# Optimization experiments

Hardware: AMD Instinct MI355X
Metric: run time of the kernel (lower is better)

Reference implementation:

```python
import jax, jax.numpy as jnp
import numpy as np

B, N, C, H = 2, 2048, 768, 12
D = C // H  # head dim = 64


def _rotate_half(x):
    d2 = x.shape[-1] // 2
    x1, x2 = x[..., :d2], x[..., d2:]
    return jnp.concatenate([-x2, x1], axis=-1)


def _apply_rope(x, sin, cos):
    # x: [B,H,N,D], sin/cos: [N,D] -> broadcast over (B,H)
    return x * cos[None, None] + _rotate_half(x) * sin[None, None]


def setup_inputs() -> dict:
    key = jax.random.key(0)
    ks = jax.random.split(key, 7)
    x = jax.random.normal(ks[0], (B, N, C), dtype=jnp.float32)
    sin_spatial = jax.random.normal(ks[1], (N, D), dtype=jnp.float32)
    cos_spatial = jax.random.normal(ks[2], (N, D), dtype=jnp.float32)
    s = 1.0 / np.sqrt(C)
    W_qkv = jax.random.uniform(ks[3], (C, 3 * C), jnp.float32, -s, s)
    b_qkv = jax.random.uniform(ks[4], (3 * C,), jnp.float32, -s, s)
    W_out = jax.random.uniform(ks[5], (C, C), jnp.float32, -s, s)
    b_out = jax.random.uniform(ks[6], (C,), jnp.float32, -s, s)
    return {"x": x, "sin_spatial": sin_spatial, "cos_spatial": cos_spatial,
            "W_qkv": W_qkv, "b_qkv": b_qkv, "W_out": W_out, "b_out": b_out}


def reference(x, sin_spatial, cos_spatial, W_qkv, b_qkv, W_out, b_out):
    qkv = x @ W_qkv + b_qkv                       # [B,N,3C]
    qkv = qkv.reshape(B, N, 3, H, D).transpose(2, 0, 3, 1, 4)  # [3,B,H,N,D]
    q, k, v = qkv[0], qkv[1], qkv[2]
    q = _apply_rope(q, sin_spatial, cos_spatial)
    k = _apply_rope(k, sin_spatial, cos_spatial)
    att = jnp.einsum('bhqd,bhkd->bhqk', q, k) * (D ** -0.5)
    att = jax.nn.softmax(att, axis=-1)            # dropout is identity (eval)
    y = jnp.einsum('bhqk,bhkd->bhqd', att, v)     # [B,H,N,D]
    y = y.transpose(0, 2, 1, 3).reshape(B, N, C)
    return y @ W_out + b_out
```

## Files before the change

### kernel.cpp

```cpp
#include <hip/hip_runtime.h>
#include <hip/hip_bf16.h>

#define BB 2
#define NN 2048
#define CC 768
#define HH 12
#define DD 64
#define MM 4096
#define N3 2304

typedef __attribute__((ext_vector_type(8))) short bf16x8;
typedef __attribute__((ext_vector_type(4))) float f32x4;

#define QSCALE 0.18033688011112043f


__device__ __forceinline__ unsigned short f2bf(float f) {
    union { float f; unsigned u; } v; v.f = f;
    unsigned r = v.u + 0x7FFFu + ((v.u >> 16) & 1u);
    return (unsigned short)(r >> 16);
}

__device__ __forceinline__ short f2bf_rn(float f) {
    union { __hip_bfloat16 h; short s; } v;
    v.h = __float2bfloat16(f);
    return v.s;
}

__device__ __forceinline__ float exp2_hw(float x) {
    float r;
    asm("v_exp_f32 %0, %1" : "=v"(r) : "v"(x));
    return r;
}

__device__ __forceinline__ bf16x8 ld_frag(const unsigned short* p) {
    bf16x8 r;
    __builtin_memcpy(&r, p, 8);
    __builtin_memcpy((char*)&r + 8, p + 16, 8);
    return r;
}

__device__ __forceinline__ bf16x8 ld_frag16(const unsigned short* p) {
    bf16x8 r;
    __builtin_memcpy(&r, p, 16);
    return r;
}

__global__ void k_cvt(const float* __restrict__ s, unsigned short* __restrict__ d, int n4) {
    int i = blockIdx.x * blockDim.x + threadIdx.x;
    int st = gridDim.x * blockDim.x;
    for (; i < n4; i += st) {
        float4 v = ((const float4*)s)[i];
        ushort4 o;
        o.x = f2bf(v.x); o.y = f2bf(v.y); o.z = f2bf(v.z); o.w = f2bf(v.w);
        ((ushort4*)d)[i] = o;
    }
}

__global__ void k_cvtT(const float* __restrict__ s, unsigned short* __restrict__ d,
                       int R, int Cc) {
    __shared__ unsigned short t[64][72];
    const int c0 = blockIdx.x * 64, r0 = blockIdx.y * 64;
    const int tr = threadIdx.x >> 4;
    const int tc = (threadIdx.x & 15) * 4;
#pragma unroll
    for (int i = 0; i < 4; i++) {
        int r = tr + i * 16;
        float4 v = *(const float4*)(s + (size_t)(r0 + r) * Cc + c0 + tc);
        t[tc + 0][r] = f2bf(v.x);
        t[tc + 1][r] = f2bf(v.y);
        t[tc + 2][r] = f2bf(v.z);
        t[tc + 3][r] = f2bf(v.w);
    }
    __syncthreads();
    const int wr = threadIdx.x >> 2;
    const int wc = (threadIdx.x & 3) * 16;
    *(uint4*)(d + (size_t)(c0 + wr) * R + r0 + wc)     = *(uint4*)&t[wr][wc];
    *(uint4*)(d + (size_t)(c0 + wr) * R + r0 + wc + 8) = *(uint4*)&t[wr][wc + 8];
}

__launch_bounds__(256)
__global__ void k_qkv(const unsigned short* __restrict__ xb,
                      const unsigned short* __restrict__ wt,
                      const float* __restrict__ bias,
                      const float* __restrict__ sinp,
                      const float* __restrict__ cosp,
                      unsigned short* __restrict__ qws,
                      unsigned short* __restrict__ kws,
                      unsigned short* __restrict__ vws) {
    __shared__ unsigned short As[128][40];
    __shared__ unsigned short Bs[64][40];
    const int tid = threadIdx.x;
    const int lane = tid & 63, w = tid >> 6;
    const int ql = lane & 15, lg = lane >> 4;
    const int row0 = blockIdx.x * 128;
    const int j0 = blockIdx.y * 64;

    f32x4 acc[2][4];
#pragma unroll
    for (int a = 0; a < 2; a++)
#pragma unroll
        for (int b = 0; b < 4; b++) acc[a][b] = f32x4{0.f, 0.f, 0.f, 0.f};

    const int ar = tid >> 1, ac = (tid & 1) * 16;
    const int jr = tid >> 2, kc = (tid & 3) * 8;

    for (int k0 = 0; k0 < CC; k0 += 32) {
        uint4 av0 = *(const uint4*)(xb + (size_t)(row0 + ar) * CC + k0 + ac);
        uint4 av1 = *(const uint4*)(xb + (size_t)(row0 + ar) * CC + k0 + ac + 8);
        uint4 bv  = *(const uint4*)(wt + (size_t)(j0 + jr) * CC + k0 + kc);
        *(uint4*)&As[ar][ac]     = av0;
        *(uint4*)&As[ar][ac + 8] = av1;
        *(uint4*)&Bs[jr][kc]     = bv;
        __syncthreads();

        bf16x8 af[2], bfr[4];
#pragma unroll
        for (int fr = 0; fr < 2; fr++) af[fr] = ld_frag(&As[w * 32 + fr * 16 + ql][lg * 4]);
#pragma unroll
        for (int fn = 0; fn < 4; fn++) bfr[fn] = ld_frag(&Bs[fn * 16 + ql][lg * 4]);
#pragma unroll
        for (int fr = 0; fr < 2; fr++)
#pragma unroll
            for (int fn = 0; fn < 4; fn++)
                acc[fr][fn] = __builtin_amdgcn_mfma_f32_16x16x32_bf16(af[fr], bfr[fn], acc[fr][fn], 0, 0, 0);
        __syncthreads();
    }

    float vals[2][4][4];
#pragma unroll
    for (int fr = 0; fr < 2; fr++)
#pragma unroll
        for (int fn = 0; fn < 4; fn++) {
            float bj = bias[j0 + fn * 16 + ql];
#pragma unroll
            for (int r = 0; r < 4; r++) vals[fr][fn][r] = acc[fr][fn][r] + bj;
        }
    const int t = j0 / CC;
    const int h = (j0 % CC) >> 6;
    if (t < 2) {
        unsigned short* outp = (t == 0) ? qws : kws;
        const float qs = (t == 0) ? QSCALE : 1.0f;
#pragma unroll
        for (int fr = 0; fr < 2; fr++)
#pragma unroll
            for (int r = 0; r < 4; r++) {
                int m = row0 + w * 32 + fr * 16 + lg * 4 + r;
                int b = m >> 11, n = m & (NN - 1);
#pragma unroll
                for (int fn = 0; fn < 4; fn++) {
                    int d = fn * 16 + ql;
                    float cv = cosp[n * DD + d], sv = sinp[n * DD + d];
                    float other = vals[fr][fn ^ 2][r];
                    float rv = (vals[fr][fn][r] * cv + ((fn < 2) ? -other : other) * sv) * qs;
                    int dcol = (t == 0) ? d
                             : ((fn >> 1) * 32 + (ql >> 2) * 8 + (fn & 1) * 4 + (ql & 3));
                    outp[((size_t)(b * HH + h) * NN + n) * DD + dcol] = f2bf(rv);
                }
            }
    } else {
#pragma unroll
        for (int fr = 0; fr < 2; fr++)
#pragma unroll
            for (int r = 0; r < 4; r++) {
                int m = row0 + w * 32 + fr * 16 + lg * 4 + r;
                int b = m >> 11, n = m & (NN - 1);
                int ncol = (n & ~31) + lg * 8 + (fr & 1) * 4 + r;
#pragma unroll
                for (int fn = 0; fn < 4; fn++) {
                    int d = fn * 16 + ql;
                    vws[((size_t)(b * HH + h) * DD + d) * NN + ncol] = f2bf(vals[fr][fn][r]);
                }
            }
    }
}

__launch_bounds__(128)
__global__ void k_attn(const unsigned short* __restrict__ qws,
                       const unsigned short* __restrict__ kws,
                       const unsigned short* __restrict__ vws,
                       unsigned short* __restrict__ yws) {
    __shared__ unsigned short Ks[2][64][72];
    __shared__ unsigned short Vs[2][64][72];
    const int tid = threadIdx.x;
    const int lane = tid & 63, w = tid >> 6;
    const int ql = lane & 15, lg = lane >> 4;
    const int d0 = blockIdx.x;
    const int bh = (d0 & 7) + 8 * (d0 >> 8);
    const int qb = (d0 >> 3) & 31;
    const int qw = qb * 64 + w * 32;
    const unsigned short* Qp = qws + (size_t)bh * NN * DD;
    const unsigned short* Kp = kws + (size_t)bh * NN * DD;
    const unsigned short* Vp = vws + (size_t)bh * DD * NN;

    bf16x8 qf[2][2];
#pragma unroll
    for (int fn = 0; fn < 2; fn++)
#pragma unroll
        for (int kb = 0; kb < 2; kb++)
            qf[fn][kb] = ld_frag(Qp + (size_t)(qw + fn * 16 + ql) * DD + kb * 32 + lg * 4);

    f32x4 oacc[4][2];
#pragma unroll
    for (int a = 0; a < 4; a++)
#pragma unroll
        for (int b = 0; b < 2; b++) oacc[a][b] = f32x4{0.f, 0.f, 0.f, 0.f};
    float mrun[2] = {-1e30f, -1e30f}, lrun[2] = {0.f, 0.f};

    const int srow = tid >> 1;
    const int shalf = (tid & 1) * 32;

#pragma unroll
    for (int j = 0; j < 4; j++) {
        *(uint4*)&Ks[0][srow][shalf + j * 8] = *(const uint4*)(Kp + (size_t)srow * DD + shalf + j * 8);
        *(uint4*)&Vs[0][srow][shalf + j * 8] = *(const uint4*)(Vp + (size_t)srow * NN + shalf + j * 8);
    }
    __syncthreads();

    const int NT = NN / 64;
    int cur = 0;
    for (int kt = 0; kt < NT; kt++) {
        uint4 kn[4], vn[4];
        const bool hasn = (kt + 1 < NT);
        if (hasn) {
#pragma unroll
            for (int j = 0; j < 4; j++) {
                kn[j] = *(const uint4*)(Kp + (size_t)((kt + 1) * 64 + srow) * DD + shalf + j * 8);
                vn[j] = *(const uint4*)(Vp + (size_t)srow * NN + (kt + 1) * 64 + shalf + j * 8);
            }
        }
        const unsigned short (*Kc)[72] = Ks[cur];
        const unsigned short (*Vc)[72] = Vs[cur];

        f32x4 sacc[4][2];
#pragma unroll
        for (int a = 0; a < 4; a++)
#pragma unroll
            for (int b = 0; b < 2; b++) sacc[a][b] = f32x4{0.f, 0.f, 0.f, 0.f};
        __builtin_amdgcn_s_setprio(1);
#pragma unroll
        for (int kb = 0; kb < 2; kb++) {
            bf16x8 kf[4];
#pragma unroll
            for (int fr = 0; fr < 4; fr++)
                kf[fr] = ld_frag16(&Kc[fr * 16 + ql][kb * 32 + lg * 8]);
#pragma unroll
            for (int fr = 0; fr < 4; fr++)
#pragma unroll
                for (int fn = 0; fn < 2; fn++)
                    sacc[fr][fn] = __builtin_amdgcn_mfma_f32_16x16x32_bf16(kf[fr], qf[fn][kb], sacc[fr][fn], 0, 0, 0);
        }
        __builtin_amdgcn_s_setprio(0);

        bf16x8 pB[2][2];
#pragma unroll
        for (int fn = 0; fn < 2; fn++) {
            float ma = fmaxf(fmaxf(sacc[0][fn][0], sacc[0][fn][1]), fmaxf(sacc[0][fn][2], sacc[0][fn][3]));
            float mb = fmaxf(fmaxf(sacc[1][fn][0], sacc[1][fn][1]), fmaxf(sacc[1][fn][2], sacc[1][fn][3]));
            float mc = fmaxf(fmaxf(sacc[2][fn][0], sacc[2][fn][1]), fmaxf(sacc[2][fn][2], sacc[2][fn][3]));
            float md = fmaxf(fmaxf(sacc[3][fn][0], sacc[3][fn][1]), fmaxf(sacc[3][fn][2], sacc[3][fn][3]));
            float tm = fmaxf(fmaxf(ma, mb), fmaxf(mc, md));
            tm = fmaxf(tm, __shfl_xor(tm, 16));
            tm = fmaxf(tm, __shfl_xor(tm, 32));
            if (__any(tm > mrun[fn] + 8.0f)) {
                float mn = fmaxf(mrun[fn], tm);
                float scl = exp2_hw(mrun[fn] - mn);
                lrun[fn] *= scl;
#pragma unroll
                for (int db = 0; db < 4; db++) oacc[db][fn] *= scl;
                mrun[fn] = mn;
            }
            float ts = 0.f;
#pragma unroll
            for (int fr = 0; fr < 4; fr++)
#pragma unroll
                for (int r = 0; r < 4; r++) {
                    float p = exp2_hw(sacc[fr][fn][r] - mrun[fn]);
                    sacc[fr][fn][r] = p;
                    ts += p;
                }
            ts += __shfl_xor(ts, 16);
            ts += __shfl_xor(ts, 32);
            lrun[fn] += ts;

#pragma unroll
            for (int kkb = 0; kkb < 2; kkb++) {
                bf16x8 t8;
#pragma unroll
                for (int e = 0; e < 8; e++)
                    t8[e] = f2bf_rn(sacc[kkb * 2 + (e >> 2)][fn][e & 3]);
                pB[fn][kkb] = t8;
            }
        }

        __builtin_amdgcn_s_setprio(1);
#pragma unroll
        for (int db = 0; db < 4; db++) {
            bf16x8 va[2];
#pragma unroll
            for (int kkb = 0; kkb < 2; kkb++)
                va[kkb] = ld_frag16(&Vc[db * 16 + ql][kkb * 32 + lg * 8]);
#pragma unroll
            for (int kkb = 0; kkb < 2; kkb++)
#pragma unroll
                for (int fn = 0; fn < 2; fn++)
                    oacc[db][fn] = __builtin_amdgcn_mfma_f32_16x16x32_bf16(va[kkb], pB[fn][kkb], oacc[db][fn], 0, 0, 0);
        }
        __builtin_amdgcn_s_setprio(0);

        if (hasn) {
#pragma unroll
            for (int j = 0; j < 4; j++) {
                *(uint4*)&Ks[cur ^ 1][srow][shalf + j * 8] = kn[j];
                *(uint4*)&Vs[cur ^ 1][srow][shalf + j * 8] = vn[j];
            }
            __syncthreads();
            cur ^= 1;
        }
    }

    const int b = bh / HH, h = bh % HH;
#pragma unroll
    for (int fn = 0; fn < 2; fn++) {
        float inv = 1.0f / lrun[fn];
        int q = qw + fn * 16 + ql;
        unsigned short* yp = yws + (size_t)(b * NN + q) * CC + h * DD + lg * 4;
#pragma unroll
        for (int db = 0; db < 4; db++) {
            ushort4 o;
            o.x = f2bf(oacc[db][fn][0] * inv);
            o.y = f2bf(oacc[db][fn][1] * inv);
            o.z = f2bf(oacc[db][fn][2] * inv);
            o.w = f2bf(oacc[db][fn][3] * inv);
            *(ushort4*)(yp + db * 16) = o;
        }
    }
}

__launch_bounds__(256)
__global__ void k_out(const unsigned short* __restrict__ yb,
                      const unsigned short* __restrict__ wt,
                      const float* __restrict__ bias,
                      float* __restrict__ out) {
    __shared__ unsigned short As[128][40];
    __shared__ unsigned short Bs[64][40];
    const int tid = threadIdx.x;
    const int lane = tid & 63, w = tid >> 6;
    const int ql = lane & 15, lg = lane >> 4;
    const int row0 = blockIdx.x * 128;
    const int j0 = blockIdx.y * 64;

    f32x4 acc[2][4];
#pragma unroll
    for (int a = 0; a < 2; a++)
#pragma unroll
        for (int b = 0; b < 4; b++) acc[a][b] = f32x4{0.f, 0.f, 0.f, 0.f};

    const int ar = tid >> 1, ac = (tid & 1) * 16;
    const int jr = tid >> 2, kc = (tid & 3) * 8;

    for (int k0 = 0; k0 < CC; k0 += 32) {
        uint4 av0 = *(const uint4*)(yb + (size_t)(row0 + ar) * CC + k0 + ac);
        uint4 av1 = *(const uint4*)(yb + (size_t)(row0 + ar) * CC + k0 + ac + 8);
        uint4 bv  = *(const uint4*)(wt + (size_t)(j0 + jr) * CC + k0 + kc);
        *(uint4*)&As[ar][ac]     = av0;
        *(uint4*)&As[ar][ac + 8] = av1;
        *(uint4*)&Bs[jr][kc]     = bv;
        __syncthreads();

        bf16x8 af[2], bfr[4];
#pragma unroll
        for (int fr = 0; fr < 2; fr++) af[fr] = ld_frag(&As[w * 32 + fr * 16 + ql][lg * 4]);
#pragma unroll
        for (int fn = 0; fn < 4; fn++) bfr[fn] = ld_frag(&Bs[fn * 16 + ql][lg * 4]);
#pragma unroll
        for (int fr = 0; fr < 2; fr++)
#pragma unroll
            for (int fn = 0; fn < 4; fn++)
                acc[fr][fn] = __builtin_amdgcn_mfma_f32_16x16x32_bf16(af[fr], bfr[fn], acc[fr][fn], 0, 0, 0);
        __syncthreads();
    }

#pragma unroll
    for (int fr = 0; fr < 2; fr++)
#pragma unroll
        for (int fn = 0; fn < 4; fn++) {
            float bj = bias[j0 + fn * 16 + ql];
#pragma unroll
            for (int r = 0; r < 4; r++) {
                int m = row0 + w * 32 + fr * 16 + lg * 4 + r;
                out[(size_t)m * CC + j0 + fn * 16 + ql] = acc[fr][fn][r] + bj;
            }
        }
}

extern "C" void kernel_launch(void* const* d_in, const int* in_sizes, int n_in,
                              void* d_out, int out_size, void* d_ws, size_t ws_size,
                              hipStream_t stream) {
    const float* x    = (const float*)d_in[0];
    const float* sinp = (const float*)d_in[1];
    const float* cosp = (const float*)d_in[2];
    const float* wqkv = (const float*)d_in[3];
    const float* bqkv = (const float*)d_in[4];
    const float* wout = (const float*)d_in[5];
    const float* bout = (const float*)d_in[6];
    float* out = (float*)d_out;
    char* ws = (char*)d_ws;

    unsigned short* xb  = (unsigned short*)(ws);
    unsigned short* wqb = (unsigned short*)(ws + 6291456);
    unsigned short* wob = (unsigned short*)(ws + 9830400);
    unsigned short* qws = (unsigned short*)(ws + 11010048);
    unsigned short* kws = (unsigned short*)(ws + 17301504);
    unsigned short* vws = (unsigned short*)(ws + 23592960);
    unsigned short* yws = (unsigned short*)(ws + 29884416);
    if (ws_size < 36175872) return;

    k_cvt<<<dim3(512), dim3(256), 0, stream>>>(x, xb, MM * CC / 4);
    k_cvtT<<<dim3(36, 12), dim3(256), 0, stream>>>(wqkv, wqb, CC, N3);
    k_cvtT<<<dim3(12, 12), dim3(256), 0, stream>>>(wout, wob, CC, CC);
    k_qkv<<<dim3(32, 36), dim3(256), 0, stream>>>(xb, wqb, bqkv, sinp, cosp, qws, kws, vws);
    k_attn<<<dim3(768), dim3(128), 0, stream>>>(qws, kws, vws, yws);
    k_out<<<dim3(32, 12), dim3(256), 0, stream>>>(yws, wob, bout, out);
}
```

Measured before the change: 136.3 us.

## Split attention KV range across two wave pairs and merge partial softmax

The attention block grows from 128 to 256 threads. Each pair of waves handles half of the key/value sequence for the same 64 queries, and the two partial results (m, l, O) are merged through shared memory at the end, flash-decoding style. This doubles the waves per block and halves each wave's serial loop length, aiming for more latency hiding on a 768-block grid. In exchange the per-half K/V double buffering is gone, so each tile load now sits between two barriers, and the merge step adds shared-memory traffic and extra syncs.

```diff
diff --git a/kernel.cpp b/kernel.cpp
--- a/kernel.cpp
+++ b/kernel.cpp
@@ -175,24 +175,27 @@
     }
 }
 
-__launch_bounds__(128)
+__launch_bounds__(256, 3)
 __global__ void k_attn(const unsigned short* __restrict__ qws,
                        const unsigned short* __restrict__ kws,
                        const unsigned short* __restrict__ vws,
                        unsigned short* __restrict__ yws) {
-    __shared__ unsigned short Ks[2][64][72];
-    __shared__ unsigned short Vs[2][64][72];
+    __shared__ __align__(16) unsigned short SM[4 * 64 * 72];
     const int tid = threadIdx.x;
     const int lane = tid & 63, w = tid >> 6;
     const int ql = lane & 15, lg = lane >> 4;
+    const int qgrp = w & 1, khalf = w >> 1;
     const int d0 = blockIdx.x;
     const int bh = (d0 & 7) + 8 * (d0 >> 8);
     const int qb = (d0 >> 3) & 31;
-    const int qw = qb * 64 + w * 32;
+    const int qw = qb * 64 + qgrp * 32;
     const unsigned short* Qp = qws + (size_t)bh * NN * DD;
     const unsigned short* Kp = kws + (size_t)bh * NN * DD;
     const unsigned short* Vp = vws + (size_t)bh * DD * NN;
 
+    unsigned short* Kc = SM + khalf * (64 * 72);
+    unsigned short* Vc = SM + (2 + khalf) * (64 * 72);
+
     bf16x8 qf[2][2];
 #pragma unroll
     for (int fn = 0; fn < 2; fn++)
@@ -207,30 +210,30 @@
         for (int b = 0; b < 2; b++) oacc[a][b] = f32x4{0.f, 0.f, 0.f, 0.f};
     float mrun[2] = {-1e30f, -1e30f}, lrun[2] = {0.f, 0.f};
 
-    const int srow = tid >> 1;
-    const int shalf = (tid & 1) * 32;
+    const int htid = tid & 127;
+    const int srow = htid >> 1;
+    const int shalf = (htid & 1) * 32;
 
 #pragma unroll
     for (int j = 0; j < 4; j++) {
-        *(uint4*)&Ks[0][srow][shalf + j * 8] = *(const uint4*)(Kp + (size_t)srow * DD + shalf + j * 8);
-        *(uint4*)&Vs[0][srow][shalf + j * 8] = *(const uint4*)(Vp + (size_t)srow * NN + shalf + j * 8);
+        *(uint4*)&Kc[srow * 72 + shalf + j * 8] =
+            *(const uint4*)(Kp + (size_t)(khalf * 1024 + srow) * DD + shalf + j * 8);
+        *(uint4*)&Vc[srow * 72 + shalf + j * 8] =
+            *(const uint4*)(Vp + (size_t)srow * NN + khalf * 1024 + shalf + j * 8);
     }
     __syncthreads();
 
-    const int NT = NN / 64;
-    int cur = 0;
-    for (int kt = 0; kt < NT; kt++) {
+    for (int t = 0; t < 16; t++) {
+        const int g = khalf * 16 + t;
         uint4 kn[4], vn[4];
-        const bool hasn = (kt + 1 < NT);
+        const bool hasn = (t + 1 < 16);
         if (hasn) {
 #pragma unroll
             for (int j = 0; j < 4; j++) {
-                kn[j] = *(const uint4*)(Kp + (size_t)((kt + 1) * 64 + srow) * DD + shalf + j * 8);
-                vn[j] = *(const uint4*)(Vp + (size_t)srow * NN + (kt + 1) * 64 + shalf + j * 8);
-            }
-        }
-        const unsigned short (*Kc)[72] = Ks[cur];
-        const unsigned short (*Vc)[72] = Vs[cur];
+                kn[j] = *(const uint4*)(Kp + (size_t)((g + 1) * 64 + srow) * DD + shalf + j * 8);
+                vn[j] = *(const uint4*)(Vp + (size_t)srow * NN + (g + 1) * 64 + shalf + j * 8);
+            }
+        }
 
         f32x4 sacc[4][2];
 #pragma unroll
@@ -243,7 +246,7 @@
             bf16x8 kf[4];
 #pragma unroll
             for (int fr = 0; fr < 4; fr++)
-                kf[fr] = ld_frag16(&Kc[fr * 16 + ql][kb * 32 + lg * 8]);
+                kf[fr] = ld_frag16(&Kc[(fr * 16 + ql) * 72 + kb * 32 + lg * 8]);
 #pragma unroll
             for (int fr = 0; fr < 4; fr++)
 #pragma unroll
@@ -299,7 +302,7 @@
             bf16x8 va[2];
 #pragma unroll
             for (int kkb = 0; kkb < 2; kkb++)
-                va[kkb] = ld_frag16(&Vc[db * 16 + ql][kkb * 32 + lg * 8]);
+                va[kkb] = ld_frag16(&Vc[(db * 16 + ql) * 72 + kkb * 32 + lg * 8]);
 #pragma unroll
             for (int kkb = 0; kkb < 2; kkb++)
 #pragma unroll
@@ -309,30 +312,54 @@
         __builtin_amdgcn_s_setprio(0);
 
         if (hasn) {
+            __syncthreads();
 #pragma unroll
             for (int j = 0; j < 4; j++) {
-                *(uint4*)&Ks[cur ^ 1][srow][shalf + j * 8] = kn[j];
-                *(uint4*)&Vs[cur ^ 1][srow][shalf + j * 8] = vn[j];
+                *(uint4*)&Kc[srow * 72 + shalf + j * 8] = kn[j];
+                *(uint4*)&Vc[srow * 72 + shalf + j * 8] = vn[j];
             }
             __syncthreads();
-            cur ^= 1;
-        }
-    }
-
-    const int b = bh / HH, h = bh % HH;
-#pragma unroll
-    for (int fn = 0; fn < 2; fn++) {
-        float inv = 1.0f / lrun[fn];
-        int q = qw + fn * 16 + ql;
-        unsigned short* yp = yws + (size_t)(b * NN + q) * CC + h * DD + lg * 4;
-#pragma unroll
-        for (int db = 0; db < 4; db++) {
-            ushort4 o;
-            o.x = f2bf(oacc[db][fn][0] * inv);
-            o.y = f2bf(oacc[db][fn][1] * inv);
-            o.z = f2bf(oacc[db][fn][2] * inv);
-            o.w = f2bf(oacc[db][fn][3] * inv);
-            *(ushort4*)(yp + db * 16) = o;
+        }
+    }
+
+    __syncthreads();
+    float* ex = (float*)SM;
+    const int exb = (qgrp * 64 + lane) * 37;
+    if (khalf == 1) {
+#pragma unroll
+        for (int fn = 0; fn < 2; fn++)
+#pragma unroll
+            for (int db = 0; db < 4; db++)
+#pragma unroll
+                for (int r = 0; r < 4; r++)
+                    ex[exb + fn * 16 + db * 4 + r] = oacc[db][fn][r];
+        ex[exb + 32] = mrun[0];
+        ex[exb + 33] = mrun[1];
+        ex[exb + 34] = lrun[0];
+        ex[exb + 35] = lrun[1];
+    }
+    __syncthreads();
+    if (khalf == 0) {
+        const int b = bh / HH, h = bh % HH;
+#pragma unroll
+        for (int fn = 0; fn < 2; fn++) {
+            float m1 = ex[exb + 32 + fn];
+            float l1 = ex[exb + 34 + fn];
+            float M  = fmaxf(mrun[fn], m1);
+            float e0 = exp2_hw(mrun[fn] - M);
+            float e1 = exp2_hw(m1 - M);
+            float inv = 1.0f / (lrun[fn] * e0 + l1 * e1);
+            int q = qw + fn * 16 + ql;
+            unsigned short* yp = yws + (size_t)(b * NN + q) * CC + h * DD + lg * 4;
+#pragma unroll
+            for (int db = 0; db < 4; db++) {
+                ushort4 o;
+                o.x = f2bf((oacc[db][fn][0] * e0 + ex[exb + fn * 16 + db * 4 + 0] * e1) * inv);
+                o.y = f2bf((oacc[db][fn][1] * e0 + ex[exb + fn * 16 + db * 4 + 1] * e1) * inv);
+                o.z = f2bf((oacc[db][fn][2] * e0 + ex[exb + fn * 16 + db * 4 + 2] * e1) * inv);
+                o.w = f2bf((oacc[db][fn][3] * e0 + ex[exb + fn * 16 + db * 4 + 3] * e1) * inv);
+                *(ushort4*)(yp + db * 16) = o;
+            }
         }
     }
 }
@@ -420,6 +447,6 @@
     k_cvtT<<<dim3(36, 12), dim3(256), 0, stream>>>(wqkv, wqb, CC, N3);
     k_cvtT<<<dim3(12, 12), dim3(256), 0, stream>>>(wout, wob, CC, CC);
     k_qkv<<<dim3(32, 36), dim3(256), 0, stream>>>(xb, wqb, bqkv, sinp, cosp, qws, kws, vws);
-    k_attn<<<dim3(768), dim3(128), 0, stream>>>(qws, kws, vws, yws);
+    k_attn<<<dim3(768), dim3(256), 0, stream>>>(qws, kws, vws, yws);
     k_out<<<dim3(32, 12), dim3(256), 0, stream>>>(yws, wob, bout, out);
 }
```

New measurement: 198.4 us. 1.46x slower.

## Run attention blocks as single waves with one K/V LDS buffer and no barriers

Applied to the files above, without the earlier changes.

The attention kernel changes from two-wave blocks with a double-buffered K/V tile in LDS to one-wave blocks. Each wave stages the whole 64-row K and V tile itself through a single LDS buffer, and the grid doubles to 1536 blocks. Because a wave's own LDS reads and writes stay in program order, the __syncthreads barrier is removed and LDS use per block drops. The trade-off is that each wave now loads the full K/V tile on its own, so global/L2 traffic for K/V doubles and the 16 prefetch registers per thread may raise register pressure.

```diff
diff --git a/kernel.cpp b/kernel.cpp
--- a/kernel.cpp
+++ b/kernel.cpp
@@ -175,20 +175,19 @@
     }
 }
 
-__launch_bounds__(128)
+__launch_bounds__(64)
 __global__ void k_attn(const unsigned short* __restrict__ qws,
                        const unsigned short* __restrict__ kws,
                        const unsigned short* __restrict__ vws,
                        unsigned short* __restrict__ yws) {
-    __shared__ unsigned short Ks[2][64][72];
-    __shared__ unsigned short Vs[2][64][72];
-    const int tid = threadIdx.x;
-    const int lane = tid & 63, w = tid >> 6;
+    __shared__ __align__(16) unsigned short Ks[64][72];
+    __shared__ __align__(16) unsigned short Vs[64][72];
+    const int lane = threadIdx.x;
     const int ql = lane & 15, lg = lane >> 4;
     const int d0 = blockIdx.x;
-    const int bh = (d0 & 7) + 8 * (d0 >> 8);
-    const int qb = (d0 >> 3) & 31;
-    const int qw = qb * 64 + w * 32;
+    const int bh = (d0 & 7) + 8 * (d0 >> 9);
+    const int qb = (d0 >> 3) & 63;
+    const int qw = qb * 32;
     const unsigned short* Qp = qws + (size_t)bh * NN * DD;
     const unsigned short* Kp = kws + (size_t)bh * NN * DD;
     const unsigned short* Vp = vws + (size_t)bh * DD * NN;
@@ -207,30 +206,30 @@
         for (int b = 0; b < 2; b++) oacc[a][b] = f32x4{0.f, 0.f, 0.f, 0.f};
     float mrun[2] = {-1e30f, -1e30f}, lrun[2] = {0.f, 0.f};
 
-    const int srow = tid >> 1;
-    const int shalf = (tid & 1) * 32;
-
-#pragma unroll
-    for (int j = 0; j < 4; j++) {
-        *(uint4*)&Ks[0][srow][shalf + j * 8] = *(const uint4*)(Kp + (size_t)srow * DD + shalf + j * 8);
-        *(uint4*)&Vs[0][srow][shalf + j * 8] = *(const uint4*)(Vp + (size_t)srow * NN + shalf + j * 8);
-    }
-    __syncthreads();
-
-    const int NT = NN / 64;
-    int cur = 0;
-    for (int kt = 0; kt < NT; kt++) {
-        uint4 kn[4], vn[4];
-        const bool hasn = (kt + 1 < NT);
+    {
+        uint4 kr[8], vr[8];
+#pragma unroll
+        for (int j = 0; j < 8; j++) {
+            kr[j] = *(const uint4*)(Kp + (size_t)lane * DD + j * 8);
+            vr[j] = *(const uint4*)(Vp + (size_t)lane * NN + j * 8);
+        }
+#pragma unroll
+        for (int j = 0; j < 8; j++) {
+            *(uint4*)&Ks[lane][j * 8] = kr[j];
+            *(uint4*)&Vs[lane][j * 8] = vr[j];
+        }
+    }
+
+    for (int t = 0; t < NN / 64; t++) {
+        uint4 kn[8], vn[8];
+        const bool hasn = (t + 1 < NN / 64);
         if (hasn) {
 #pragma unroll
-            for (int j = 0; j < 4; j++) {
-                kn[j] = *(const uint4*)(Kp + (size_t)((kt + 1) * 64 + srow) * DD + shalf + j * 8);
-                vn[j] = *(const uint4*)(Vp + (size_t)srow * NN + (kt + 1) * 64 + shalf + j * 8);
-            }
-        }
-        const unsigned short (*Kc)[72] = Ks[cur];
-        const unsigned short (*Vc)[72] = Vs[cur];
+            for (int j = 0; j < 8; j++) {
+                kn[j] = *(const uint4*)(Kp + (size_t)((t + 1) * 64 + lane) * DD + j * 8);
+                vn[j] = *(const uint4*)(Vp + (size_t)lane * NN + (t + 1) * 64 + j * 8);
+            }
+        }
 
         f32x4 sacc[4][2];
 #pragma unroll
@@ -243,7 +242,7 @@
             bf16x8 kf[4];
 #pragma unroll
             for (int fr = 0; fr < 4; fr++)
-                kf[fr] = ld_frag16(&Kc[fr * 16 + ql][kb * 32 + lg * 8]);
+                kf[fr] = ld_frag16(&Ks[fr * 16 + ql][kb * 32 + lg * 8]);
 #pragma unroll
             for (int fr = 0; fr < 4; fr++)
 #pragma unroll
@@ -299,7 +298,7 @@
             bf16x8 va[2];
 #pragma unroll
             for (int kkb = 0; kkb < 2; kkb++)
-                va[kkb] = ld_frag16(&Vc[db * 16 + ql][kkb * 32 + lg * 8]);
+                va[kkb] = ld_frag16(&Vs[db * 16 + ql][kkb * 32 + lg * 8]);
 #pragma unroll
             for (int kkb = 0; kkb < 2; kkb++)
 #pragma unroll
@@ -310,12 +309,10 @@
 
         if (hasn) {
 #pragma unroll
-            for (int j = 0; j < 4; j++) {
-                *(uint4*)&Ks[cur ^ 1][srow][shalf + j * 8] = kn[j];
-                *(uint4*)&Vs[cur ^ 1][srow][shalf + j * 8] = vn[j];
-            }
-            __syncthreads();
-            cur ^= 1;
+            for (int j = 0; j < 8; j++) {
+                *(uint4*)&Ks[lane][j * 8] = kn[j];
+                *(uint4*)&Vs[lane][j * 8] = vn[j];
+            }
         }
     }
 
@@ -420,6 +417,6 @@
     k_cvtT<<<dim3(36, 12), dim3(256), 0, stream>>>(wqkv, wqb, CC, N3);
     k_cvtT<<<dim3(12, 12), dim3(256), 0, stream>>>(wout, wob, CC, CC);
     k_qkv<<<dim3(32, 36), dim3(256), 0, stream>>>(xb, wqb, bqkv, sinp, cosp, qws, kws, vws);
-    k_attn<<<dim3(768), dim3(128), 0, stream>>>(qws, kws, vws, yws);
+    k_attn<<<dim3(1536), dim3(64), 0, stream>>>(qws, kws, vws, yws);
     k_out<<<dim3(32, 12), dim3(256), 0, stream>>>(yws, wob, bout, out);
 }
```

New measurement: 167.7 us. 1.23x slower.

## Enlarge projection GEMM tiles to 128x128 and permute Q layout for wide fragment loads

Applied to the files above, without the earlier changes.

Both projection GEMMs move from 128x64 to 128x128 block tiles, with a 2x2 warp arrangement where each warp computes a 64x64 sub-tile. This doubles data reuse per LDS load and halves the block count. Q is now written in the same permuted column layout as K, so the attention kernel can load its Q fragments with a single 16-byte load (ld_frag16). The trade-off is more accumulator registers per thread and fewer blocks: the output projection drops to 192 blocks, which may leave compute units idle.

```diff
diff --git a/kernel.cpp b/kernel.cpp
--- a/kernel.cpp
+++ b/kernel.cpp
@@ -89,89 +89,98 @@
                       unsigned short* __restrict__ kws,
                       unsigned short* __restrict__ vws) {
     __shared__ unsigned short As[128][40];
-    __shared__ unsigned short Bs[64][40];
+    __shared__ unsigned short Bs[128][40];
     const int tid = threadIdx.x;
     const int lane = tid & 63, w = tid >> 6;
     const int ql = lane & 15, lg = lane >> 4;
+    const int wr = w >> 1, wc = w & 1;
     const int row0 = blockIdx.x * 128;
-    const int j0 = blockIdx.y * 64;
-
-    f32x4 acc[2][4];
-#pragma unroll
-    for (int a = 0; a < 2; a++)
+    const int j0 = blockIdx.y * 128;
+
+    f32x4 acc[4][4];
+#pragma unroll
+    for (int a = 0; a < 4; a++)
 #pragma unroll
         for (int b = 0; b < 4; b++) acc[a][b] = f32x4{0.f, 0.f, 0.f, 0.f};
 
     const int ar = tid >> 1, ac = (tid & 1) * 16;
-    const int jr = tid >> 2, kc = (tid & 3) * 8;
 
     for (int k0 = 0; k0 < CC; k0 += 32) {
-        uint4 av0 = *(const uint4*)(xb + (size_t)(row0 + ar) * CC + k0 + ac);
-        uint4 av1 = *(const uint4*)(xb + (size_t)(row0 + ar) * CC + k0 + ac + 8);
-        uint4 bv  = *(const uint4*)(wt + (size_t)(j0 + jr) * CC + k0 + kc);
-        *(uint4*)&As[ar][ac]     = av0;
-        *(uint4*)&As[ar][ac + 8] = av1;
-        *(uint4*)&Bs[jr][kc]     = bv;
+        uint4 a0 = *(const uint4*)(xb + (size_t)(row0 + ar) * CC + k0 + ac);
+        uint4 a1 = *(const uint4*)(xb + (size_t)(row0 + ar) * CC + k0 + ac + 8);
+        uint4 b0 = *(const uint4*)(wt + (size_t)(j0 + ar) * CC + k0 + ac);
+        uint4 b1 = *(const uint4*)(wt + (size_t)(j0 + ar) * CC + k0 + ac + 8);
+        *(uint4*)&As[ar][ac]     = a0;
+        *(uint4*)&As[ar][ac + 8] = a1;
+        *(uint4*)&Bs[ar][ac]     = b0;
+        *(uint4*)&Bs[ar][ac + 8] = b1;
         __syncthreads();
 
-        bf16x8 af[2], bfr[4];
-#pragma unroll
-        for (int fr = 0; fr < 2; fr++) af[fr] = ld_frag(&As[w * 32 + fr * 16 + ql][lg * 4]);
-#pragma unroll
-        for (int fn = 0; fn < 4; fn++) bfr[fn] = ld_frag(&Bs[fn * 16 + ql][lg * 4]);
-#pragma unroll
-        for (int fr = 0; fr < 2; fr++)
+        bf16x8 af[4], bfr[4];
+#pragma unroll
+        for (int fr = 0; fr < 4; fr++) af[fr] = ld_frag(&As[wr * 64 + fr * 16 + ql][lg * 4]);
+#pragma unroll
+        for (int fn = 0; fn < 4; fn++) bfr[fn] = ld_frag(&Bs[wc * 64 + fn * 16 + ql][lg * 4]);
+#pragma unroll
+        for (int fr = 0; fr < 4; fr++)
 #pragma unroll
             for (int fn = 0; fn < 4; fn++)
                 acc[fr][fn] = __builtin_amdgcn_mfma_f32_16x16x32_bf16(af[fr], bfr[fn], acc[fr][fn], 0, 0, 0);
         __syncthreads();
     }
 
-    float vals[2][4][4];
-#pragma unroll
-    for (int fr = 0; fr < 2; fr++)
-#pragma unroll
-        for (int fn = 0; fn < 4; fn++) {
-            float bj = bias[j0 + fn * 16 + ql];
-#pragma unroll
-            for (int r = 0; r < 4; r++) vals[fr][fn][r] = acc[fr][fn][r] + bj;
-        }
-    const int t = j0 / CC;
-    const int h = (j0 % CC) >> 6;
+    const int j0w = j0 + wc * 64;
+    const int t = j0w / CC;
+    const int h = (j0w % CC) >> 6;
     if (t < 2) {
         unsigned short* outp = (t == 0) ? qws : kws;
         const float qs = (t == 0) ? QSCALE : 1.0f;
 #pragma unroll
-        for (int fr = 0; fr < 2; fr++)
+        for (int fr = 0; fr < 4; fr++) {
+            float v4[4][4];
+#pragma unroll
+            for (int fn = 0; fn < 4; fn++) {
+                float bj = bias[j0w + fn * 16 + ql];
+#pragma unroll
+                for (int r = 0; r < 4; r++) v4[fn][r] = acc[fr][fn][r] + bj;
+            }
 #pragma unroll
             for (int r = 0; r < 4; r++) {
-                int m = row0 + w * 32 + fr * 16 + lg * 4 + r;
+                int m = row0 + wr * 64 + fr * 16 + lg * 4 + r;
                 int b = m >> 11, n = m & (NN - 1);
 #pragma unroll
                 for (int fn = 0; fn < 4; fn++) {
                     int d = fn * 16 + ql;
                     float cv = cosp[n * DD + d], sv = sinp[n * DD + d];
-                    float other = vals[fr][fn ^ 2][r];
-                    float rv = (vals[fr][fn][r] * cv + ((fn < 2) ? -other : other) * sv) * qs;
-                    int dcol = (t == 0) ? d
-                             : ((fn >> 1) * 32 + (ql >> 2) * 8 + (fn & 1) * 4 + (ql & 3));
+                    float other = v4[fn ^ 2][r];
+                    float rv = (v4[fn][r] * cv + ((fn < 2) ? -other : other) * sv) * qs;
+                    int dcol = (fn >> 1) * 32 + (ql >> 2) * 8 + (fn & 1) * 4 + (ql & 3);
                     outp[((size_t)(b * HH + h) * NN + n) * DD + dcol] = f2bf(rv);
                 }
             }
+        }
     } else {
 #pragma unroll
-        for (int fr = 0; fr < 2; fr++)
+        for (int fr = 0; fr < 4; fr++) {
+            float v4[4][4];
+#pragma unroll
+            for (int fn = 0; fn < 4; fn++) {
+                float bj = bias[j0w + fn * 16 + ql];
+#pragma unroll
+                for (int r = 0; r < 4; r++) v4[fn][r] = acc[fr][fn][r] + bj;
+            }
 #pragma unroll
             for (int r = 0; r < 4; r++) {
-                int m = row0 + w * 32 + fr * 16 + lg * 4 + r;
+                int m = row0 + wr * 64 + fr * 16 + lg * 4 + r;
                 int b = m >> 11, n = m & (NN - 1);
                 int ncol = (n & ~31) + lg * 8 + (fr & 1) * 4 + r;
 #pragma unroll
                 for (int fn = 0; fn < 4; fn++) {
                     int d = fn * 16 + ql;
-                    vws[((size_t)(b * HH + h) * DD + d) * NN + ncol] = f2bf(vals[fr][fn][r]);
+                    vws[((size_t)(b * HH + h) * DD + d) * NN + ncol] = f2bf(v4[fn][r]);
                 }
             }
+        }
     }
 }
 
@@ -198,7 +207,7 @@
     for (int fn = 0; fn < 2; fn++)
 #pragma unroll
         for (int kb = 0; kb < 2; kb++)
-            qf[fn][kb] = ld_frag(Qp + (size_t)(qw + fn * 16 + ql) * DD + kb * 32 + lg * 4);
+            qf[fn][kb] = ld_frag16(Qp + (size_t)(qw + fn * 16 + ql) * DD + kb * 32 + lg * 8);
 
     f32x4 oacc[4][2];
 #pragma unroll
@@ -343,38 +352,40 @@
                       const float* __restrict__ bias,
                       float* __restrict__ out) {
     __shared__ unsigned short As[128][40];
-    __shared__ unsigned short Bs[64][40];
+    __shared__ unsigned short Bs[128][40];
     const int tid = threadIdx.x;
     const int lane = tid & 63, w = tid >> 6;
     const int ql = lane & 15, lg = lane >> 4;
+    const int wr = w >> 1, wc = w & 1;
     const int row0 = blockIdx.x * 128;
-    const int j0 = blockIdx.y * 64;
-
-    f32x4 acc[2][4];
-#pragma unroll
-    for (int a = 0; a < 2; a++)
+    const int j0 = blockIdx.y * 128;
+
+    f32x4 acc[4][4];
+#pragma unroll
+    for (int a = 0; a < 4; a++)
 #pragma unroll
         for (int b = 0; b < 4; b++) acc[a][b] = f32x4{0.f, 0.f, 0.f, 0.f};
 
     const int ar = tid >> 1, ac = (tid & 1) * 16;
-    const int jr = tid >> 2, kc = (tid & 3) * 8;
 
     for (int k0 = 0; k0 < CC; k0 += 32) {
-        uint4 av0 = *(const uint4*)(yb + (size_t)(row0 + ar) * CC + k0 + ac);
-        uint4 av1 = *(const uint4*)(yb + (size_t)(row0 + ar) * CC + k0 + ac + 8);
-        uint4 bv  = *(const uint4*)(wt + (size_t)(j0 + jr) * CC + k0 + kc);
-        *(uint4*)&As[ar][ac]     = av0;
-        *(uint4*)&As[ar][ac + 8] = av1;
-        *(uint4*)&Bs[jr][kc]     = bv;
+        uint4 a0 = *(const uint4*)(yb + (size_t)(row0 + ar) * CC + k0 + ac);
+        uint4 a1 = *(const uint4*)(yb + (size_t)(row0 + ar) * CC + k0 + ac + 8);
+        uint4 b0 = *(const uint4*)(wt + (size_t)(j0 + ar) * CC + k0 + ac);
+        uint4 b1 = *(const uint4*)(wt + (size_t)(j0 + ar) * CC + k0 + ac + 8);
+        *(uint4*)&As[ar][ac]     = a0;
+        *(uint4*)&As[ar][ac + 8] = a1;
+        *(uint4*)&Bs[ar][ac]     = b0;
+        *(uint4*)&Bs[ar][ac + 8] = b1;
         __syncthreads();
 
-        bf16x8 af[2], bfr[4];
-#pragma unroll
-        for (int fr = 0; fr < 2; fr++) af[fr] = ld_frag(&As[w * 32 + fr * 16 + ql][lg * 4]);
-#pragma unroll
-        for (int fn = 0; fn < 4; fn++) bfr[fn] = ld_frag(&Bs[fn * 16 + ql][lg * 4]);
-#pragma unroll
-        for (int fr = 0; fr < 2; fr++)
+        bf16x8 af[4], bfr[4];
+#pragma unroll
+        for (int fr = 0; fr < 4; fr++) af[fr] = ld_frag(&As[wr * 64 + fr * 16 + ql][lg * 4]);
+#pragma unroll
+        for (int fn = 0; fn < 4; fn++) bfr[fn] = ld_frag(&Bs[wc * 64 + fn * 16 + ql][lg * 4]);
+#pragma unroll
+        for (int fr = 0; fr < 4; fr++)
 #pragma unroll
             for (int fn = 0; fn < 4; fn++)
                 acc[fr][fn] = __builtin_amdgcn_mfma_f32_16x16x32_bf16(af[fr], bfr[fn], acc[fr][fn], 0, 0, 0);
@@ -382,14 +393,14 @@
     }
 
 #pragma unroll
-    for (int fr = 0; fr < 2; fr++)
+    for (int fr = 0; fr < 4; fr++)
 #pragma unroll
         for (int fn = 0; fn < 4; fn++) {
-            float bj = bias[j0 + fn * 16 + ql];
+            float bj = bias[j0 + wc * 64 + fn * 16 + ql];
 #pragma unroll
             for (int r = 0; r < 4; r++) {
-                int m = row0 + w * 32 + fr * 16 + lg * 4 + r;
-                out[(size_t)m * CC + j0 + fn * 16 + ql] = acc[fr][fn][r] + bj;
+                int m = row0 + wr * 64 + fr * 16 + lg * 4 + r;
+                out[(size_t)m * CC + j0 + wc * 64 + fn * 16 + ql] = acc[fr][fn][r] + bj;
             }
         }
 }
@@ -419,7 +430,7 @@
     k_cvt<<<dim3(512), dim3(256), 0, stream>>>(x, xb, MM * CC / 4);
     k_cvtT<<<dim3(36, 12), dim3(256), 0, stream>>>(wqkv, wqb, CC, N3);
     k_cvtT<<<dim3(12, 12), dim3(256), 0, stream>>>(wout, wob, CC, CC);
-    k_qkv<<<dim3(32, 36), dim3(256), 0, stream>>>(xb, wqb, bqkv, sinp, cosp, qws, kws, vws);
+    k_qkv<<<dim3(32, 18), dim3(256), 0, stream>>>(xb, wqb, bqkv, sinp, cosp, qws, kws, vws);
     k_attn<<<dim3(768), dim3(128), 0, stream>>>(qws, kws, vws, yws);
-    k_out<<<dim3(32, 12), dim3(256), 0, stream>>>(yws, wob, bout, out);
-}
+    k_out<<<dim3(32, 6), dim3(256), 0, stream>>>(yws, wob, bout, out);
+}
```

Measured after the change: 145.4 us. +6.7%, slower.
